# Optimization experiments

Measured on AMD Instinct MI355X. Metric: run time of the kernel, lower is better.

Reference implementation:

```python
import jax, jax.numpy as jnp
import numpy as np

TOP_K = 16  # config.top_k


def setup_inputs() -> dict:
    key = jax.random.key(0)
    k1, k2 = jax.random.split(key)
    B, L, D = 32, 4096, 768
    T = 2048  # num_topics
    x = jax.random.normal(k1, (B, L, D), dtype=jnp.float32)
    topic_vectors = jax.random.normal(k2, (T, D), dtype=jnp.float32)
    return {"x": x, "topic_vectors": topic_vectors}


def reference(x, topic_vectors):
    B, L, D = x.shape
    T = topic_vectors.shape[0]
    # softmax over word dimension, then top-k indices per topic
    dist = jax.nn.softmax(topic_vectors, axis=1)            # [T, D]
    top_idx = jax.lax.top_k(dist, TOP_K)[1] % L             # [T, K], in [0, L)
    # One vectorized scatter replaces the torch triple loop. The pattern is
    # identical for every batch element, so build [L, T] once and broadcast.
    cols = jnp.arange(T, dtype=top_idx.dtype)[:, None]      # [T, 1] -> broadcasts to [T, K]
    hg2d = jnp.zeros((L, T), dtype=x.dtype).at[top_idx, cols].set(1.0)
    hypergraph = jnp.broadcast_to(hg2d[None], (B, L, T))    # [B, L, T]
    return hypergraph
```

## Files before the change

### kernel.cpp

```cpp
#include <hip/hip_runtime.h>
#include <hip/hip_bf16.h>
#include <stdint.h>


#define B_DIM    32
#define L_DIM    4096
#define D_DIM    768
#define T_TOPICS 2048
#define K_TOP    16

#define WORDS_PER_ROW (T_TOPICS / 32)
#define BITMAP_WORDS  (D_DIM * WORDS_PER_ROW)

__global__ void zero_bitmap_kernel(uint32_t* __restrict__ bm) {
    int i = blockIdx.x * blockDim.x + threadIdx.x;
    if (i < BITMAP_WORDS) bm[i] = 0u;
}

__global__ void topk_kernel(const float* __restrict__ tv, uint32_t* __restrict__ bm) {
    const int t    = blockIdx.x;
    const int lane = threadIdx.x;
    const float* __restrict__ row = tv + (size_t)t * D_DIM;

    float v[D_DIM / 64];
    #pragma unroll
    for (int j = 0; j < D_DIM / 64; ++j) v[j] = row[lane + j * 64];

    for (int k = 0; k < K_TOP; ++k) {
        float bv = v[0];
        int   bj = 0;
        #pragma unroll
        for (int j = 1; j < D_DIM / 64; ++j) {
            if (v[j] > bv) { bv = v[j]; bj = j; }
        }
        float cv = bv;
        int   ci = lane + bj * 64;
        #pragma unroll
        for (int off = 32; off > 0; off >>= 1) {
            float ov = __shfl_xor(cv, off);
            int   oi = __shfl_xor(ci, off);
            if (ov > cv || (ov == cv && oi < ci)) { cv = ov; ci = oi; }
        }
        if ((ci & 63) == lane) v[ci >> 6] = -INFINITY;
        if (lane == 0) {
            atomicOr(&bm[ci * WORDS_PER_ROW + (t >> 5)], 1u << (t & 31));
        }
    }
}

__global__ void fill_kernel(const uint32_t* __restrict__ bm, float4* __restrict__ out) {
    const unsigned total  = (unsigned)B_DIM * L_DIM * (T_TOPICS / 4);
    const unsigned stride = gridDim.x * blockDim.x;
    for (unsigned q = blockIdx.x * blockDim.x + threadIdx.x; q < total; q += stride) {
        const int t4 = (int)(q & (T_TOPICS / 4 - 1));
        const int l  = (int)((q >> 9) & (L_DIM - 1));
        uint32_t w = 0u;
        if (l < D_DIM) w = bm[l * WORDS_PER_ROW + (t4 >> 3)];
        const int sh = (t4 & 7) * 4;
        float4 val;
        val.x = ((w >> (sh + 0)) & 1u) ? 1.0f : 0.0f;
        val.y = ((w >> (sh + 1)) & 1u) ? 1.0f : 0.0f;
        val.z = ((w >> (sh + 2)) & 1u) ? 1.0f : 0.0f;
        val.w = ((w >> (sh + 3)) & 1u) ? 1.0f : 0.0f;
        out[q] = val;
    }
}

extern "C" void kernel_launch(void* const* d_in, const int* in_sizes, int n_in,
                              void* d_out, int out_size, void* d_ws, size_t ws_size,
                              hipStream_t stream) {
    const float* tv  = (const float*)d_in[1];
    float*       out = (float*)d_out;
    uint32_t*    bm  = (uint32_t*)d_ws;

    hipLaunchKernelGGL(zero_bitmap_kernel,
                       dim3((BITMAP_WORDS + 255) / 256), dim3(256), 0, stream, bm);
    hipLaunchKernelGGL(topk_kernel,
                       dim3(T_TOPICS), dim3(64), 0, stream, tv, bm);
    hipLaunchKernelGGL(fill_kernel,
                       dim3(2048), dim3(256), 0, stream, bm, (float4*)out);
}
```

Baseline: 220.1 us.

## Zero output with memset and scatter only nonzero bitmap words

Replaces the full-output fill kernel with hipMemsetAsync to zero the whole output, followed by a sparse kernel. That kernel visits only rows l < D for each batch and writes float4 groups only where the bitmap word is nonzero. The aim is to let the driver's memset handle the bulk of the zero writes and to avoid computing and storing zeros from a custom kernel. Nonzero regions are written twice, and the change adds a memset launch and relies on out_size being in floats.

```diff
diff --git a/kernel.cpp b/kernel.cpp
--- a/kernel.cpp
+++ b/kernel.cpp
@@ -11,6 +11,9 @@
 
 #define WORDS_PER_ROW (T_TOPICS / 32)
 #define BITMAP_WORDS  (D_DIM * WORDS_PER_ROW)
+#define PLANE_F  (L_DIM * T_TOPICS)
+
+typedef float f32x4 __attribute__((ext_vector_type(4)));
 
 __global__ void zero_bitmap_kernel(uint32_t* __restrict__ bm) {
     int i = blockIdx.x * blockDim.x + threadIdx.x;
@@ -48,21 +51,28 @@
     }
 }
 
-__global__ void fill_kernel(const uint32_t* __restrict__ bm, float4* __restrict__ out) {
-    const unsigned total  = (unsigned)B_DIM * L_DIM * (T_TOPICS / 4);
-    const unsigned stride = gridDim.x * blockDim.x;
-    for (unsigned q = blockIdx.x * blockDim.x + threadIdx.x; q < total; q += stride) {
-        const int t4 = (int)(q & (T_TOPICS / 4 - 1));
-        const int l  = (int)((q >> 9) & (L_DIM - 1));
-        uint32_t w = 0u;
-        if (l < D_DIM) w = bm[l * WORDS_PER_ROW + (t4 >> 3)];
-        const int sh = (t4 & 7) * 4;
-        float4 val;
-        val.x = ((w >> (sh + 0)) & 1u) ? 1.0f : 0.0f;
-        val.y = ((w >> (sh + 1)) & 1u) ? 1.0f : 0.0f;
-        val.z = ((w >> (sh + 2)) & 1u) ? 1.0f : 0.0f;
-        val.w = ((w >> (sh + 3)) & 1u) ? 1.0f : 0.0f;
-        out[q] = val;
+__global__ __launch_bounds__(256) void rewrite_kernel(const uint32_t* __restrict__ bm,
+                                                      float* __restrict__ out) {
+    const unsigned W    = blockIdx.x * 4u + (threadIdx.x >> 6);
+    const unsigned lane = threadIdx.x & 63u;
+    const unsigned wg8  = W & 7u;
+    const unsigned r    = W >> 3;
+    const unsigned l    = r % (unsigned)D_DIM;
+    const unsigned b    = r / (unsigned)D_DIM;
+
+    const unsigned word_idx = wg8 * 8u + (lane >> 3);
+    const uint32_t w = bm[l * WORDS_PER_ROW + word_idx];
+    if (w != 0u) {
+        const unsigned s    = lane & 7u;
+        const unsigned bits = (w >> (s * 4u)) & 0xFu;
+        f32x4 val;
+        val.x = (bits & 1u) ? 1.0f : 0.0f;
+        val.y = (bits & 2u) ? 1.0f : 0.0f;
+        val.z = (bits & 4u) ? 1.0f : 0.0f;
+        val.w = (bits & 8u) ? 1.0f : 0.0f;
+        float* p = out + (size_t)b * PLANE_F + (size_t)l * T_TOPICS
+                       + word_idx * 32u + s * 4u;
+        *(f32x4*)p = val;
     }
 }
 
@@ -77,6 +87,10 @@
                        dim3((BITMAP_WORDS + 255) / 256), dim3(256), 0, stream, bm);
     hipLaunchKernelGGL(topk_kernel,
                        dim3(T_TOPICS), dim3(64), 0, stream, tv, bm);
-    hipLaunchKernelGGL(fill_kernel,
-                       dim3(2048), dim3(256), 0, stream, bm, (float4*)out);
+
+    hipMemsetAsync(d_out, 0, (size_t)out_size * sizeof(float), stream);
+
+    const unsigned total_waves = (unsigned)D_DIM * B_DIM * 8u;
+    hipLaunchKernelGGL(rewrite_kernel,
+                       dim3(total_waves / 4), dim3(256), 0, stream, bm, out);
 }
```

New measurement: 220.1 us. About the same (+0.0%).
